# Kernel optimization log

Measured on AMD Instinct MI355X. Metric: run time of the kernel, lower is better.

The kernel has to match this reference:

```python
import jax, jax.numpy as jnp
import numpy as np

D_MODEL = 1024
N_HEADS = 16
D_K = D_MODEL // N_HEADS


def setup_inputs() -> dict:
    key = jax.random.key(0)
    kx, kq, kk, kv, ko = jax.random.split(key, 5)
    s = 1.0 / np.sqrt(D_MODEL)
    return {
        "x": jax.random.normal(kx, (4, 2048, D_MODEL), dtype=jnp.float32),
        "W_q": jax.random.normal(kq, (D_MODEL, D_MODEL), dtype=jnp.float32) * s,
        "W_k": jax.random.normal(kk, (D_MODEL, D_MODEL), dtype=jnp.float32) * s,
        "W_v": jax.random.normal(kv, (D_MODEL, D_MODEL), dtype=jnp.float32) * s,
        "W_o": jax.random.normal(ko, (D_MODEL, D_MODEL), dtype=jnp.float32) * s,
    }


def reference(x, W_q, W_k, W_v, W_o):
    B, S, _ = x.shape
    # torch nn.Linear computes x @ W.T; our W_* stored as [out, in]-equivalent square,
    # use plain x @ W (equivalent parameterization for a random weight).
    def split_heads(t):  # [B,S,D] -> [B,H,S,d_k]
        return t.reshape(B, S, N_HEADS, D_K).transpose(0, 2, 1, 3)

    Q = split_heads(x @ W_q)
    K = split_heads(x @ W_k)
    V = split_heads(x @ W_v)
    scale = 1.0 / np.sqrt(D_K).astype(np.float32)
    scores = jnp.einsum('bhqd,bhkd->bhqk', Q, K) * scale  # [B,H,S,S]
    causal_mask = jnp.tril(jnp.ones((S, S), dtype=bool))  # True = keep
    scores = jnp.where(causal_mask, scores, jnp.float32(-jnp.inf))
    attn = jax.nn.softmax(scores, axis=-1)
    out = jnp.einsum('bhqk,bhkd->bhqd', attn, V)  # [B,H,S,d_k]
    out = out.transpose(0, 2, 1, 3).reshape(B, S, D_MODEL)
    return out @ W_o
```

## Files before the change

### kernel.cpp

```cpp
#include <hip/hip_runtime.h>
#include <hip/hip_bf16.h>
#include <stdint.h>

#define B_SZ 4
#define SEQ 2048
#define DM 1024
#define NH 16
#define DK 64
#define BH (B_SZ * NH)
#define M_TOT (B_SZ * SEQ)

typedef unsigned short u16;
typedef u16 u16x8 __attribute__((ext_vector_type(8)));
typedef __bf16 bf16x8 __attribute__((ext_vector_type(8)));
typedef float f32x4 __attribute__((ext_vector_type(4)));

__device__ __forceinline__ u16 f2bf(float f) {
    union { float f; uint32_t u; } v; v.f = f;
    uint32_t u = v.u;
    return (u16)((u + 0x7FFFu + ((u >> 16) & 1u)) >> 16);
}

__device__ __forceinline__ u16 f2bf_trunc(float f) {
    union { float f; uint32_t u; } v; v.f = f;
    return (u16)(v.u >> 16);
}

__device__ __forceinline__ f32x4 mfma16(u16x8 a, u16x8 b, f32x4 c) {
    return __builtin_amdgcn_mfma_f32_16x16x32_bf16(
        __builtin_bit_cast(bf16x8, a), __builtin_bit_cast(bf16x8, b), c, 0, 0, 0);
}

__device__ __forceinline__ void gload16_lds(const void* g, void* l) {
    __builtin_amdgcn_global_load_lds(
        (const __attribute__((address_space(1))) void*)(uintptr_t)g,
        (__attribute__((address_space(3))) void*)(uintptr_t)l, 16, 0, 0);
}

__global__ void cvt_bf16_kernel(const float* __restrict__ in, u16* __restrict__ out, int n4) {
    int i = blockIdx.x * blockDim.x + threadIdx.x;
    if (i < n4) {
        float4 v = ((const float4*)in)[i];
        ushort4 o;
        o.x = f2bf(v.x); o.y = f2bf(v.y); o.z = f2bf(v.z); o.w = f2bf(v.w);
        ((ushort4*)out)[i] = o;
    }
}

__global__ void transpose_w_kernel(const float* __restrict__ W0, const float* __restrict__ W1,
                                   u16* __restrict__ Wt) {
    __shared__ u16 tile[32][33];
    int bx = blockIdx.x, by = blockIdx.y, z = blockIdx.z;
    const float* W = z ? W1 : W0;
    u16* Wd = Wt + (size_t)z * DM * DM;
    int t = threadIdx.x;
    for (int i = 0; i < 4; i++) {
        int idx = t + i * 256;
        int r = idx >> 5, c = idx & 31;
        tile[r][c] = f2bf(W[(by * 32 + r) * DM + bx * 32 + c]);
    }
    __syncthreads();
    for (int i = 0; i < 4; i++) {
        int idx = t + i * 256;
        int r2 = idx >> 5, c2 = idx & 31;
        Wd[(bx * 32 + r2) * DM + by * 32 + c2] = tile[c2][r2];
    }
}

template <int AFP32, int MODE>
__global__ __launch_bounds__(256, 2) void gemm128(
    const void* __restrict__ Ain, const u16* __restrict__ Bt,
    void* __restrict__ C0p, void* __restrict__ C1p, float scale0) {
    __shared__ u16 As[128][32];
    __shared__ u16 Bs[128][32];
    const int K = DM;
    int m0 = blockIdx.x * 128;
    int n0 = blockIdx.y * 128;
    int tid = threadIdx.x;
    int lane = tid & 63, wave = tid >> 6;
    int quad = lane >> 4, l15 = lane & 15;
    int wm = wave >> 1, wn = wave & 1;

    f32x4 acc[4][4];
    for (int i = 0; i < 4; i++)
        for (int j = 0; j < 4; j++) acc[i][j] = f32x4{0.f, 0.f, 0.f, 0.f};

    int rS = lane >> 2;
    int cS = (lane & 3) * 8;

    for (int k0 = 0; k0 < K; k0 += 32) {
        __syncthreads();
        if (AFP32) {
            const float* A = (const float*)Ain;
            for (int i = 0; i < 4; i++) {
                int idx = tid + i * 256;
                int r = idx >> 3, c = (idx & 7) * 4;
                float4 v = *(const float4*)(&A[(size_t)(m0 + r) * K + k0 + c]);
                ushort4 o;
                o.x = f2bf(v.x); o.y = f2bf(v.y); o.z = f2bf(v.z); o.w = f2bf(v.w);
                *(ushort4*)(&As[r][c]) = o;
            }
        } else {
            const u16* A = (const u16*)Ain;
            const u16* ga = &A[(size_t)(m0 + wave * 32 + rS) * K + k0 + cS];
            gload16_lds(ga, &As[wave * 32][0]);
            gload16_lds(ga + (size_t)16 * K, &As[wave * 32 + 16][0]);
        }
        {
            const u16* gb = &Bt[(size_t)(n0 + wave * 32 + rS) * K + k0 + cS];
            gload16_lds(gb, &Bs[wave * 32][0]);
            gload16_lds(gb + (size_t)16 * K, &Bs[wave * 32 + 16][0]);
        }
        __syncthreads();
        u16x8 af[4], bfv[4];
        for (int mt = 0; mt < 4; mt++)
            af[mt] = *(const u16x8*)(&As[wm * 64 + mt * 16 + l15][quad * 8]);
        for (int nt = 0; nt < 4; nt++)
            bfv[nt] = *(const u16x8*)(&Bs[wn * 64 + nt * 16 + l15][quad * 8]);
        for (int mt = 0; mt < 4; mt++)
            for (int nt = 0; nt < 4; nt++)
                acc[mt][nt] = mfma16(af[mt], bfv[nt], acc[mt][nt]);
    }

    for (int mt = 0; mt < 4; mt++)
        for (int nt = 0; nt < 4; nt++)
            for (int r = 0; r < 4; r++) {
                int m = m0 + wm * 64 + mt * 16 + quad * 4 + r;
                int n = n0 + wn * 64 + nt * 16 + l15;
                float v = acc[mt][nt][r];
                if (MODE == 0) {
                    v *= (n < 1024) ? scale0 : 1.0f;
                    u16* C = (n < 1024) ? (u16*)C0p : (u16*)C1p;
                    int ne = n & 1023;
                    int b = m >> 11, s = m & 2047;
                    int h = ne >> 6, d = ne & 63;
                    C[(((size_t)(b * NH + h) * SEQ) + s) * DK + d] = f2bf(v);
                } else if (MODE == 1) {
                    ((float*)C0p)[(size_t)m * DM + n] = v;
                } else {
                    int b = m >> 11, s = m & 2047;
                    int h = n >> 6, d = n & 63;
                    ((u16*)C0p)[(((size_t)(b * NH + h) * DK) + d) * SEQ + s] = f2bf(v);
                }
            }
}

__global__ __launch_bounds__(256, 3) void attn_kernel(
    const u16* __restrict__ Qb, const u16* __restrict__ Kb,
    const u16* __restrict__ Vtb, u16* __restrict__ AOb) {
    __shared__ u16 Kl[2][64][64];
    __shared__ u16 Vl[2][64][64];
    __shared__ u16 Pl[4][32][64];

    int bh = blockIdx.x;
    int qs = 15 - blockIdx.y;
    int q0 = qs * 128;
    int tid = threadIdx.x, lane = tid & 63, wave = tid >> 6;
    int quad = lane >> 4, l15 = lane & 15;
    int b = bh >> 4, h = bh & 15;

    const u16* Qg = Qb + (size_t)bh * SEQ * DK;
    const u16* Kg = Kb + (size_t)bh * SEQ * DK;
    const u16* Vg = Vtb + (size_t)bh * DK * SEQ;

    int rw = lane >> 3;
    int gsw = (lane & 7) ^ rw;
    int sw8 = l15 & 7;
    u16* Pw = &Pl[wave][0][0];

    u16x8 aq[2][2];
    for (int g = 0; g < 2; g++)
        for (int kc = 0; kc < 2; kc++)
            aq[g][kc] = *(const u16x8*)(
                &Qg[(size_t)(q0 + wave * 32 + g * 16 + l15) * DK + kc * 32 + quad * 8]);

    float lsum[2][4];
    f32x4 O[2][4];
    for (int g = 0; g < 2; g++)
        for (int r = 0; r < 4; r++) lsum[g][r] = 0.f;
    for (int g = 0; g < 2; g++)
        for (int nt = 0; nt < 4; nt++) O[g][nt] = f32x4{0.f, 0.f, 0.f, 0.f};

    {
        const u16* gk = &Kg[(size_t)(wave * 16 + rw) * DK + gsw * 8];
        gload16_lds(gk, &Kl[0][wave * 16][0]);
        gload16_lds(gk + 8 * DK, &Kl[0][wave * 16 + 8][0]);
        const u16* gv = &Vg[(size_t)(wave * 16 + rw) * SEQ + gsw * 8];
        gload16_lds(gv, &Vl[0][wave * 16][0]);
        gload16_lds(gv + 8 * SEQ, &Vl[0][wave * 16 + 8][0]);
    }
    __syncthreads();

    int nkt = 2 * qs + 2;
    int lastkt = 2 * qs + (wave >> 1);
    int buf = 0;
    for (int kt = 0; kt < nkt; kt++) {
        if (kt + 1 < nkt) {
            int k0n = (kt + 1) * 64;
            const u16* gk = &Kg[(size_t)(k0n + wave * 16 + rw) * DK + gsw * 8];
            gload16_lds(gk, &Kl[buf ^ 1][wave * 16][0]);
            gload16_lds(gk + 8 * DK, &Kl[buf ^ 1][wave * 16 + 8][0]);
            const u16* gv = &Vg[(size_t)(wave * 16 + rw) * SEQ + k0n + gsw * 8];
            gload16_lds(gv, &Vl[buf ^ 1][wave * 16][0]);
            gload16_lds(gv + 8 * SEQ, &Vl[buf ^ 1][wave * 16 + 8][0]);
        }

        if (kt <= lastkt) {
            bool diag = (kt == lastkt);
            f32x4 sc[2][4];
            __builtin_amdgcn_s_setprio(1);
            #pragma unroll
            for (int nt = 0; nt < 4; nt++) {
                const u16* kr = &Kl[buf][nt * 16 + l15][0];
                u16x8 b0 = *(const u16x8*)(kr + (quad ^ sw8) * 8);
                u16x8 b1 = *(const u16x8*)(kr + ((4 + quad) ^ sw8) * 8);
                #pragma unroll
                for (int g = 0; g < 2; g++) {
                    f32x4 z = f32x4{0.f, 0.f, 0.f, 0.f};
                    z = mfma16(aq[g][0], b0, z);
                    z = mfma16(aq[g][1], b1, z);
                    sc[g][nt] = z;
                }
            }
            __builtin_amdgcn_s_setprio(0);
            #pragma unroll
            for (int g = 0; g < 2; g++) {
                if (diag) {
                    #pragma unroll
                    for (int nt = 0; nt < 4; nt++)
                        #pragma unroll
                        for (int r = 0; r < 4; r++) {
                            int qq = q0 + wave * 32 + g * 16 + quad * 4 + r;
                            int kk = kt * 64 + nt * 16 + l15;
                            float e = exp2f(sc[g][nt][r]);
                            float pv = (kk <= qq) ? e : 0.f;
                            sc[g][nt][r] = pv;
                            lsum[g][r] += pv;
                        }
                } else {
                    #pragma unroll
                    for (int nt = 0; nt < 4; nt++)
                        #pragma unroll
                        for (int r = 0; r < 4; r++) {
                            float pv = exp2f(sc[g][nt][r]);
                            sc[g][nt][r] = pv;
                            lsum[g][r] += pv;
                        }
                }
                #pragma unroll
                for (int nt = 0; nt < 4; nt++)
                    #pragma unroll
                    for (int r = 0; r < 4; r++) {
                        int prow = g * 16 + quad * 4 + r;
                        int pcol = nt * 16 + l15;
                        int scol = (((pcol >> 3) ^ (prow & 7)) << 3) | (pcol & 7);
                        Pw[prow * 64 + scol] = f2bf_trunc(sc[g][nt][r]);
                    }
            }
            u16x8 ap[2][2];
            #pragma unroll
            for (int g = 0; g < 2; g++)
                #pragma unroll
                for (int kc = 0; kc < 2; kc++)
                    ap[g][kc] = *(const u16x8*)(
                        &Pw[(g * 16 + l15) * 64 + (((kc * 4 + quad) ^ sw8) << 3)]);
            __builtin_amdgcn_s_setprio(1);
            #pragma unroll
            for (int nt = 0; nt < 4; nt++) {
                const u16* vr = &Vl[buf][nt * 16 + l15][0];
                u16x8 b0 = *(const u16x8*)(vr + (quad ^ sw8) * 8);
                u16x8 b1 = *(const u16x8*)(vr + ((4 + quad) ^ sw8) * 8);
                #pragma unroll
                for (int g = 0; g < 2; g++) {
                    O[g][nt] = mfma16(ap[g][0], b0, O[g][nt]);
                    O[g][nt] = mfma16(ap[g][1], b1, O[g][nt]);
                }
            }
            __builtin_amdgcn_s_setprio(0);
        }
        __syncthreads();
        buf ^= 1;
    }

    #pragma unroll
    for (int g = 0; g < 2; g++)
        #pragma unroll
        for (int r = 0; r < 4; r++) {
            float s = lsum[g][r];
            for (int off = 1; off < 16; off <<= 1) s += __shfl_xor(s, off, 64);
            float inv = 1.0f / s;
            int q = q0 + wave * 32 + g * 16 + quad * 4 + r;
            #pragma unroll
            for (int nt = 0; nt < 4; nt++) {
                int d = nt * 16 + l15;
                AOb[((size_t)(b * SEQ + q)) * DM + h * DK + d] = f2bf(O[g][nt][r] * inv);
            }
        }
}

extern "C" void kernel_launch(void* const* d_in, const int* in_sizes, int n_in,
                              void* d_out, int out_size, void* d_ws, size_t ws_size,
                              hipStream_t stream) {
    const float* x = (const float*)d_in[0];
    const float* Wq = (const float*)d_in[1];
    const float* Wk = (const float*)d_in[2];
    const float* Wv = (const float*)d_in[3];
    const float* Wo = (const float*)d_in[4];
    float* out = (float*)d_out;

    const size_t HALF = (size_t)M_TOT * DM * 2;
    char* S0 = (char*)d_ws;
    char* S1 = (char*)d_ws + HALF;
    char* D0 = (char*)d_out;
    char* D1 = (char*)d_out + HALF;

    u16* xb  = (u16*)S0;
    u16* Qb  = (u16*)S1;
    u16* Kb  = (u16*)D1;
    u16* Vt  = (u16*)D0;
    u16* AOb = (u16*)S0;
    u16* wqk = (u16*)D0;
    u16* wvt = (u16*)S0;
    u16* wot = (u16*)S1;

    const float cscale = 0.125f * 1.44269504088896f;
    dim3 tg2(32, 32, 2);
    dim3 tg1(32, 32, 1);
    dim3 gg(M_TOT / 128, DM / 128);

    int n4 = M_TOT * DM / 4;
    cvt_bf16_kernel<<<n4 / 256, 256, 0, stream>>>(x, xb, n4);

    transpose_w_kernel<<<tg2, 256, 0, stream>>>(Wq, Wk, wqk);
    dim3 gqk(M_TOT / 128, 2048 / 128);
    gemm128<0, 0><<<gqk, 256, 0, stream>>>(xb, wqk, (void*)Qb, (void*)Kb, cscale);

    transpose_w_kernel<<<tg1, 256, 0, stream>>>(Wv, Wv, wvt);
    gemm128<1, 2><<<gg, 256, 0, stream>>>(x, wvt, (void*)Vt, (void*)Vt, 1.0f);

    dim3 ag(BH, 16);
    attn_kernel<<<ag, 256, 0, stream>>>(Qb, Kb, Vt, AOb);

    transpose_w_kernel<<<tg1, 256, 0, stream>>>(Wo, Wo, wot);
    gemm128<0, 1><<<gg, 256, 0, stream>>>(AOb, wot, (void*)out, (void*)out, 1.0f);
}
```

Before: 266.9 us.

## Load K/V tiles directly from global into registers, dropping LDS staging and barriers

The attention kernel no longer stages K and V tiles through double-buffered shared memory with block-wide barriers. Each wave now loads its K and V fragments straight from global memory into registers, prefetching the next tile after the current MFMAs, and each wave stops at its own causal limit. This removes the __syncthreads and LDS traffic, but every wave reads K/V separately (4x redundant global/L2 traffic), register pressure rises, and occupancy is reduced to 2 blocks. The P conversion also switches from truncation to a hardware bf16 cast with rounding.

After: 339.3 us. 1.27x slower.

```diff
diff --git a/kernel.cpp b/kernel.cpp
--- a/kernel.cpp
+++ b/kernel.cpp
@@ -16,14 +16,7 @@
 typedef float f32x4 __attribute__((ext_vector_type(4)));
 
 __device__ __forceinline__ u16 f2bf(float f) {
-    union { float f; uint32_t u; } v; v.f = f;
-    uint32_t u = v.u;
-    return (u16)((u + 0x7FFFu + ((u >> 16) & 1u)) >> 16);
-}
-
-__device__ __forceinline__ u16 f2bf_trunc(float f) {
-    union { float f; uint32_t u; } v; v.f = f;
-    return (u16)(v.u >> 16);
+    return __builtin_bit_cast(u16, (__bf16)f);
 }
 
 __device__ __forceinline__ f32x4 mfma16(u16x8 a, u16x8 b, f32x4 c) {
@@ -145,11 +138,9 @@
             }
 }
 
-__global__ __launch_bounds__(256, 3) void attn_kernel(
+__global__ __launch_bounds__(256, 2) void attn_kernel(
     const u16* __restrict__ Qb, const u16* __restrict__ Kb,
     const u16* __restrict__ Vtb, u16* __restrict__ AOb) {
-    __shared__ u16 Kl[2][64][64];
-    __shared__ u16 Vl[2][64][64];
     __shared__ u16 Pl[4][32][64];
 
     int bh = blockIdx.x;
@@ -163,123 +154,126 @@
     const u16* Kg = Kb + (size_t)bh * SEQ * DK;
     const u16* Vg = Vtb + (size_t)bh * DK * SEQ;
 
-    int rw = lane >> 3;
-    int gsw = (lane & 7) ^ rw;
     int sw8 = l15 & 7;
     u16* Pw = &Pl[wave][0][0];
 
     u16x8 aq[2][2];
+    #pragma unroll
     for (int g = 0; g < 2; g++)
+        #pragma unroll
         for (int kc = 0; kc < 2; kc++)
             aq[g][kc] = *(const u16x8*)(
                 &Qg[(size_t)(q0 + wave * 32 + g * 16 + l15) * DK + kc * 32 + quad * 8]);
 
     float lsum[2][4];
     f32x4 O[2][4];
+    #pragma unroll
     for (int g = 0; g < 2; g++)
+        #pragma unroll
         for (int r = 0; r < 4; r++) lsum[g][r] = 0.f;
+    #pragma unroll
     for (int g = 0; g < 2; g++)
+        #pragma unroll
         for (int nt = 0; nt < 4; nt++) O[g][nt] = f32x4{0.f, 0.f, 0.f, 0.f};
 
-    {
-        const u16* gk = &Kg[(size_t)(wave * 16 + rw) * DK + gsw * 8];
-        gload16_lds(gk, &Kl[0][wave * 16][0]);
-        gload16_lds(gk + 8 * DK, &Kl[0][wave * 16 + 8][0]);
-        const u16* gv = &Vg[(size_t)(wave * 16 + rw) * SEQ + gsw * 8];
-        gload16_lds(gv, &Vl[0][wave * 16][0]);
-        gload16_lds(gv + 8 * SEQ, &Vl[0][wave * 16 + 8][0]);
-    }
-    __syncthreads();
-
-    int nkt = 2 * qs + 2;
     int lastkt = 2 * qs + (wave >> 1);
-    int buf = 0;
-    for (int kt = 0; kt < nkt; kt++) {
-        if (kt + 1 < nkt) {
-            int k0n = (kt + 1) * 64;
-            const u16* gk = &Kg[(size_t)(k0n + wave * 16 + rw) * DK + gsw * 8];
-            gload16_lds(gk, &Kl[buf ^ 1][wave * 16][0]);
-            gload16_lds(gk + 8 * DK, &Kl[buf ^ 1][wave * 16 + 8][0]);
-            const u16* gv = &Vg[(size_t)(wave * 16 + rw) * SEQ + k0n + gsw * 8];
-            gload16_lds(gv, &Vl[buf ^ 1][wave * 16][0]);
-            gload16_lds(gv + 8 * SEQ, &Vl[buf ^ 1][wave * 16 + 8][0]);
-        }
-
-        if (kt <= lastkt) {
-            bool diag = (kt == lastkt);
-            f32x4 sc[2][4];
-            __builtin_amdgcn_s_setprio(1);
-            #pragma unroll
-            for (int nt = 0; nt < 4; nt++) {
-                const u16* kr = &Kl[buf][nt * 16 + l15][0];
-                u16x8 b0 = *(const u16x8*)(kr + (quad ^ sw8) * 8);
-                u16x8 b1 = *(const u16x8*)(kr + ((4 + quad) ^ sw8) * 8);
-                #pragma unroll
-                for (int g = 0; g < 2; g++) {
-                    f32x4 z = f32x4{0.f, 0.f, 0.f, 0.f};
-                    z = mfma16(aq[g][0], b0, z);
-                    z = mfma16(aq[g][1], b1, z);
-                    sc[g][nt] = z;
-                }
-            }
-            __builtin_amdgcn_s_setprio(0);
-            #pragma unroll
-            for (int g = 0; g < 2; g++) {
-                if (diag) {
-                    #pragma unroll
-                    for (int nt = 0; nt < 4; nt++)
-                        #pragma unroll
-                        for (int r = 0; r < 4; r++) {
-                            int qq = q0 + wave * 32 + g * 16 + quad * 4 + r;
-                            int kk = kt * 64 + nt * 16 + l15;
-                            float e = exp2f(sc[g][nt][r]);
-                            float pv = (kk <= qq) ? e : 0.f;
-                            sc[g][nt][r] = pv;
-                            lsum[g][r] += pv;
-                        }
-                } else {
-                    #pragma unroll
-                    for (int nt = 0; nt < 4; nt++)
-                        #pragma unroll
-                        for (int r = 0; r < 4; r++) {
-                            float pv = exp2f(sc[g][nt][r]);
-                            sc[g][nt][r] = pv;
-                            lsum[g][r] += pv;
-                        }
-                }
+
+    u16x8 kb0[4], kb1[4], vb0[4], vb1[4];
+    #pragma unroll
+    for (int nt = 0; nt < 4; nt++) {
+        const u16* kr = &Kg[(size_t)(nt * 16 + l15) * DK + quad * 8];
+        kb0[nt] = *(const u16x8*)kr;
+        kb1[nt] = *(const u16x8*)(kr + 32);
+        const u16* vr = &Vg[(size_t)(nt * 16 + l15) * SEQ + quad * 8];
+        vb0[nt] = *(const u16x8*)vr;
+        vb1[nt] = *(const u16x8*)(vr + 32);
+    }
+
+    for (int kt = 0; kt <= lastkt; kt++) {
+        bool diag = (kt == lastkt);
+        int knext = diag ? kt : kt + 1;
+        int k0n = knext * 64;
+
+        f32x4 sc[2][4];
+        __builtin_amdgcn_s_setprio(1);
+        #pragma unroll
+        for (int nt = 0; nt < 4; nt++) {
+            f32x4 z0 = f32x4{0.f, 0.f, 0.f, 0.f};
+            f32x4 z1 = f32x4{0.f, 0.f, 0.f, 0.f};
+            z0 = mfma16(aq[0][0], kb0[nt], z0);
+            z0 = mfma16(aq[0][1], kb1[nt], z0);
+            z1 = mfma16(aq[1][0], kb0[nt], z1);
+            z1 = mfma16(aq[1][1], kb1[nt], z1);
+            sc[0][nt] = z0;
+            sc[1][nt] = z1;
+        }
+        __builtin_amdgcn_s_setprio(0);
+
+        #pragma unroll
+        for (int nt = 0; nt < 4; nt++) {
+            const u16* kr = &Kg[(size_t)(k0n + nt * 16 + l15) * DK + quad * 8];
+            kb0[nt] = *(const u16x8*)kr;
+            kb1[nt] = *(const u16x8*)(kr + 32);
+        }
+
+        #pragma unroll
+        for (int g = 0; g < 2; g++) {
+            if (diag) {
                 #pragma unroll
                 for (int nt = 0; nt < 4; nt++)
                     #pragma unroll
                     for (int r = 0; r < 4; r++) {
-                        int prow = g * 16 + quad * 4 + r;
-                        int pcol = nt * 16 + l15;
-                        int scol = (((pcol >> 3) ^ (prow & 7)) << 3) | (pcol & 7);
-                        Pw[prow * 64 + scol] = f2bf_trunc(sc[g][nt][r]);
+                        int qq = q0 + wave * 32 + g * 16 + quad * 4 + r;
+                        int kk = kt * 64 + nt * 16 + l15;
+                        float e = exp2f(sc[g][nt][r]);
+                        float pv = (kk <= qq) ? e : 0.f;
+                        sc[g][nt][r] = pv;
+                        lsum[g][r] += pv;
+                    }
+            } else {
+                #pragma unroll
+                for (int nt = 0; nt < 4; nt++)
+                    #pragma unroll
+                    for (int r = 0; r < 4; r++) {
+                        float pv = exp2f(sc[g][nt][r]);
+                        sc[g][nt][r] = pv;
+                        lsum[g][r] += pv;
                     }
             }
-            u16x8 ap[2][2];
             #pragma unroll
-            for (int g = 0; g < 2; g++)
+            for (int nt = 0; nt < 4; nt++)
                 #pragma unroll
-                for (int kc = 0; kc < 2; kc++)
-                    ap[g][kc] = *(const u16x8*)(
-                        &Pw[(g * 16 + l15) * 64 + (((kc * 4 + quad) ^ sw8) << 3)]);
-            __builtin_amdgcn_s_setprio(1);
+                for (int r = 0; r < 4; r++) {
+                    int prow = g * 16 + quad * 4 + r;
+                    int pcol = nt * 16 + l15;
+                    int scol = (((pcol >> 3) ^ (prow & 7)) << 3) | (pcol & 7);
+                    Pw[prow * 64 + scol] = f2bf(sc[g][nt][r]);
+                }
+        }
+
+        u16x8 ap[2][2];
+        #pragma unroll
+        for (int g = 0; g < 2; g++)
             #pragma unroll
-            for (int nt = 0; nt < 4; nt++) {
-                const u16* vr = &Vl[buf][nt * 16 + l15][0];
-                u16x8 b0 = *(const u16x8*)(vr + (quad ^ sw8) * 8);
-                u16x8 b1 = *(const u16x8*)(vr + ((4 + quad) ^ sw8) * 8);
-                #pragma unroll
-                for (int g = 0; g < 2; g++) {
-                    O[g][nt] = mfma16(ap[g][0], b0, O[g][nt]);
-                    O[g][nt] = mfma16(ap[g][1], b1, O[g][nt]);
-                }
-            }
-            __builtin_amdgcn_s_setprio(0);
-        }
-        __syncthreads();
-        buf ^= 1;
+            for (int kc = 0; kc < 2; kc++)
+                ap[g][kc] = *(const u16x8*)(
+                    &Pw[(g * 16 + l15) * 64 + (((kc * 4 + quad) ^ sw8) << 3)]);
+        __builtin_amdgcn_s_setprio(1);
+        #pragma unroll
+        for (int nt = 0; nt < 4; nt++) {
+            O[0][nt] = mfma16(ap[0][0], vb0[nt], O[0][nt]);
+            O[0][nt] = mfma16(ap[0][1], vb1[nt], O[0][nt]);
+            O[1][nt] = mfma16(ap[1][0], vb0[nt], O[1][nt]);
+            O[1][nt] = mfma16(ap[1][1], vb1[nt], O[1][nt]);
+        }
+        __builtin_amdgcn_s_setprio(0);
+
+        #pragma unroll
+        for (int nt = 0; nt < 4; nt++) {
+            const u16* vr = &Vg[(size_t)(nt * 16 + l15) * SEQ + k0n + quad * 8];
+            vb0[nt] = *(const u16x8*)vr;
+            vb1[nt] = *(const u16x8*)(vr + 32);
+        }
     }
 
     #pragma unroll
```
